# Optimization experiments

Hardware: AMD Instinct MI355X
Metric: run time of the kernel (lower is better)

Reference implementation:

```python
import jax, jax.numpy as jnp
import numpy as np

D = 1024        # d_model
H = 16          # n_heads
DF = 4096       # d_ff
MAXL = 1024     # max_len
MAXSTEPS = 24   # max_steps


def setup_inputs() -> dict:
    key = jax.random.key(0)
    ks = jax.random.split(key, 10)
    B, S = 4, 1024
    s = 0.02
    f32 = jnp.float32
    return {
        "x": jax.random.normal(ks[0], (B, S, D), f32),
        "original_input": jax.random.normal(ks[1], (B, S, D), f32),
        "think_step": 5,
        "step_embed": jax.random.normal(ks[2], (MAXSTEPS, D), f32) * s,
        "Wqkv": jax.random.normal(ks[3], (D, 3 * D), f32) * s,
        "bqkv": jnp.zeros((3 * D,), f32),
        "Wout": jax.random.normal(ks[4], (D, D), f32) * s,
        "bout": jnp.zeros((D,), f32),
        "Wg": jax.random.normal(ks[5], (2 * D, D), f32) * s,
        "bg": jnp.zeros((D,), f32),
        "rel_pos_bias": jax.random.normal(ks[6], (2 * MAXL - 1,), f32) * s,
        "W1": jax.random.normal(ks[7], (D, DF), f32) * s,
        "b1": jnp.zeros((DF,), f32),
        "W2": jax.random.normal(ks[8], (DF, D), f32) * s,
        "b2": jnp.zeros((D,), f32),
        "ln1_g": jnp.ones((D,), f32),
        "ln1_b": jnp.zeros((D,), f32),
        "ln2_g": jnp.ones((D,), f32),
        "ln2_b": jnp.zeros((D,), f32),
    }


def _layer_norm(x, g, b, eps=1e-5):
    m = jnp.mean(x, axis=-1, keepdims=True)
    v = jnp.mean((x - m) ** 2, axis=-1, keepdims=True)
    return (x - m) * jax.lax.rsqrt(v + eps) * g + b


def reference(x, original_input, think_step, step_embed, Wqkv, bqkv, Wout, bout,
              Wg, bg, rel_pos_bias, W1, b1, W2, b2, ln1_g, ln1_b, ln2_g, ln2_b):
    B, S, _ = x.shape
    hd = D // H
    # gated residual input injection
    gate = jax.nn.sigmoid(jnp.concatenate([x, original_input], axis=-1) @ Wg + bg)
    x = x * (1.0 - gate) + original_input * gate
    # think-step embedding (clamped)
    step = min(int(think_step), MAXSTEPS - 1)
    x = x + step_embed[step][None, None, :]
    # qkv projection -> (3, B, H, S, hd)
    qkv = (x @ Wqkv + bqkv).reshape(B, S, 3, H, hd).transpose(2, 0, 3, 1, 4)
    q, k, v = qkv[0], qkv[1], qkv[2]
    scores = jnp.einsum('bhqd,bhkd->bhqk', q, k) * (hd ** -0.5)
    # relative position bias: dist clamped to [0, 2*MAXL-2]
    pos = jnp.arange(S)
    rel = jnp.clip(pos[:, None] - pos[None, :] + (MAXL - 1), 0, 2 * MAXL - 2)
    scores = scores + rel_pos_bias[rel][None, None]  # (B,H,S,S)
    probs = jax.nn.softmax(scores, axis=-1)
    attn = jnp.einsum('bhqk,bhkd->bhqd', probs, v)
    attn = attn.transpose(0, 2, 1, 3).reshape(B, S, D)
    attn = attn @ Wout + bout
    x = _layer_norm(x + attn, ln1_g, ln1_b)
    h = jax.nn.gelu(x @ W1 + b1, approximate=False) @ W2 + b2
    return _layer_norm(x + h, ln2_g, ln2_b)
```

## Files before the change

### kernel.cpp

```cpp
#include <hip/hip_runtime.h>
#include <hip/hip_bf16.h>
#include <math.h>

#define D_MODEL 1024
#define NH      16
#define HD      64
#define DFF     4096
#define SEQ     1024
#define BATCH   4
#define TOK     (BATCH*SEQ)
#define MAXSTEPS 24

typedef __hip_bfloat16 bf16;
typedef __attribute__((ext_vector_type(8))) short short8;
typedef __attribute__((ext_vector_type(4))) float floatx4;

__device__ __forceinline__ float b2f(bf16 v){ return __bfloat162float(v); }
__device__ __forceinline__ bf16  f2b(float v){ return __float2bfloat16(v); }

__device__ __forceinline__ void gload_lds16(const bf16* g, bf16* l){
    __builtin_amdgcn_global_load_lds((const __attribute__((address_space(1))) void*)g,
                                     (__attribute__((address_space(3))) void*)l, 16, 0, 0);
}

template<int TN, int EPI>
__global__ __launch_bounds__(256)
void mfma_gemm(const bf16* __restrict__ A, const bf16* __restrict__ Bt,
               const float* __restrict__ bias, void* __restrict__ outv,
               int M, int N, int K)
{
    constexpr int NT = TN / 32;
    __shared__ bf16 As[128 * 32];
    __shared__ bf16 Bs[TN * 32];
    const int tid  = threadIdx.x;
    const int lane = tid & 63;
    const int w    = tid >> 6;
    const int wm   = w & 1, wn = w >> 1;
    const int fr   = lane & 15;
    const int q    = lane >> 4;
    const int row0 = blockIdx.y * 128, col0 = blockIdx.x * TN;

    floatx4 acc[4][NT] = {};

    for (int k0 = 0; k0 < K; k0 += 32) {
        __syncthreads();
        #pragma unroll
        for (int p = 0; p < 2; ++p) {
            int s  = p * 256 + tid;
            int m  = s >> 2;
            int qg = (s & 3) ^ ((m >> 1) & 3);
            gload_lds16(A + (size_t)(row0 + m) * K + k0 + qg * 8, As + (size_t)s * 8);
        }
        #pragma unroll
        for (int p = 0; p < TN / 64; ++p) {
            int s  = p * 256 + tid;
            int m  = s >> 2;
            int qg = (s & 3) ^ ((m >> 1) & 3);
            gload_lds16(Bt + (size_t)(col0 + m) * K + k0 + qg * 8, Bs + (size_t)s * 8);
        }
        __syncthreads();

        short8 af[4], bfg[NT];
        #pragma unroll
        for (int t = 0; t < 4; ++t) {
            int ml = wm * 64 + t * 16 + fr;
            af[t]  = *(const short8*)(As + (size_t)(ml * 4 + (q ^ ((ml >> 1) & 3))) * 8);
        }
        #pragma unroll
        for (int t = 0; t < NT; ++t) {
            int nl = wn * (TN / 2) + t * 16 + fr;
            bfg[t] = *(const short8*)(Bs + (size_t)(nl * 4 + (q ^ ((nl >> 1) & 3))) * 8);
        }
        #pragma unroll
        for (int i = 0; i < 4; ++i)
            #pragma unroll
            for (int j = 0; j < NT; ++j)
                acc[i][j] = __builtin_amdgcn_mfma_f32_16x16x32_bf16(af[i], bfg[j], acc[i][j], 0, 0, 0);
    }

    float bv[NT];
    #pragma unroll
    for (int nt = 0; nt < NT; ++nt) bv[nt] = bias[col0 + wn * (TN / 2) + nt * 16 + fr];
    #pragma unroll
    for (int mt = 0; mt < 4; ++mt) {
        #pragma unroll
        for (int nt = 0; nt < NT; ++nt) {
            int col = col0 + wn * (TN / 2) + nt * 16 + fr;
            #pragma unroll
            for (int r = 0; r < 4; ++r) {
                int row = row0 + wm * 64 + mt * 16 + q * 4 + r;
                float v = acc[mt][nt][r] + bv[nt];
                if (EPI == 0) {
                    ((float*)outv)[(size_t)row * N + col] = v;
                } else if (EPI == 1) {
                    ((bf16*)outv)[(size_t)row * N + col] = f2b(v);
                } else {
                    float g = 0.5f * v * (1.0f + erff(v * 0.70710678118654752f));
                    ((bf16*)outv)[(size_t)row * N + col] = f2b(g);
                }
            }
        }
    }
}

__global__ __launch_bounds__(256)
void transpose_kernel(const float* __restrict__ W, bf16* __restrict__ WT,
                      int K, int N)
{
    __shared__ float t[32][33];
    const int tx = threadIdx.x & 31, ty = threadIdx.x >> 5;
    const int n0 = blockIdx.x * 32, k0 = blockIdx.y * 32;
    #pragma unroll
    for (int i = 0; i < 4; ++i)
        t[ty + i * 8][tx] = W[(size_t)(k0 + ty + i * 8) * N + n0 + tx];
    __syncthreads();
    #pragma unroll
    for (int i = 0; i < 4; ++i)
        WT[(size_t)(n0 + ty + i * 8) * K + k0 + tx] = f2b(t[tx][ty + i * 8]);
}

__global__ __launch_bounds__(256)
void vtrans_kernel(const bf16* __restrict__ qkv, bf16* __restrict__ Vt)
{
    __shared__ float t[32][33];
    const int blk = blockIdx.x;
    const int dt = blk & 1;
    const int st = (blk >> 1) & 31;
    const int h  = (blk >> 6) & 15;
    const int b  = blk >> 10;
    const int tx = threadIdx.x & 31, ty = threadIdx.x >> 5;
    #pragma unroll
    for (int i = 0; i < 4; ++i)
        t[ty + i * 8][tx] = b2f(qkv[(size_t)(b * SEQ + st * 32 + ty + i * 8) * 3072
                                    + 2048 + h * 64 + dt * 32 + tx]);
    __syncthreads();
    #pragma unroll
    for (int i = 0; i < 4; ++i)
        Vt[(size_t)((b * NH + h) * 64 + dt * 32 + ty + i * 8) * SEQ + st * 32 + tx]
            = f2b(t[tx][ty + i * 8]);
}

__global__ __launch_bounds__(256)
void xcat_kernel(const float* __restrict__ x, const float* __restrict__ orig,
                 bf16* __restrict__ xcat)
{
    int i = blockIdx.x * 256 + threadIdx.x;
    float4 xv = ((const float4*)x)[i];
    float4 ov = ((const float4*)orig)[i];
    int t = i >> 8, c4 = (i & 255) * 4;
    bf16* px = xcat + (size_t)t * 2048 + c4;
    px[0] = f2b(xv.x); px[1] = f2b(xv.y); px[2] = f2b(xv.z); px[3] = f2b(xv.w);
    bf16* po = px + 1024;
    po[0] = f2b(ov.x); po[1] = f2b(ov.y); po[2] = f2b(ov.z); po[3] = f2b(ov.w);
}

__global__ __launch_bounds__(256)
void gatemix_kernel(const float* __restrict__ x, const float* __restrict__ orig,
                    const float* __restrict__ z, const int* __restrict__ step_ptr,
                    const float* __restrict__ se, bf16* __restrict__ xw)
{
    int i = blockIdx.x * 256 + threadIdx.x;
    int st = step_ptr[0];
    st = st < 0 ? 0 : (st > MAXSTEPS - 1 ? MAXSTEPS - 1 : st);
    float g = 1.0f / (1.0f + expf(-z[i]));
    float v = x[i] * (1.0f - g) + orig[i] * g + se[st * D_MODEL + (i & 1023)];
    xw[i] = f2b(v);
}

__global__ __launch_bounds__(256)
void fattn_kernel(const bf16* __restrict__ qkv, const bf16* __restrict__ Vt,
                  const float* __restrict__ relb, bf16* __restrict__ out)
{
    __shared__ bf16 KPs[128 * 64];
    __shared__ bf16 Vs [64 * 128];

    const int tid  = threadIdx.x;
    const int lane = tid & 63;
    const int w    = tid >> 6;
    const int fr   = lane & 15;
    const int quad = lane >> 4;

    const int qt = blockIdx.x & 15;
    const int h  = (blockIdx.x >> 4) & 15;
    const int b  = blockIdx.x >> 8;
    const int bq = b * SEQ;
    const int bh = b * NH + h;

    const int qrow = bq + qt * 64 + w * 16 + fr;
    short8 qf[2];
    {
        const bf16* qp = qkv + (size_t)qrow * 3072 + h * 64 + quad * 8;
        qf[0] = *(const short8*)(qp);
        qf[1] = *(const short8*)(qp + 32);
    }

    float m_run[4], l_run[4];
    floatx4 accO[4];
    #pragma unroll
    for (int r = 0; r < 4; ++r) { m_run[r] = -1e30f; l_run[r] = 0.f; }
    #pragma unroll
    for (int nt = 0; nt < 4; ++nt) accO[nt] = (floatx4){0.f, 0.f, 0.f, 0.f};

    for (int k0 = 0; k0 < SEQ; k0 += 128) {
        __syncthreads();
        #pragma unroll
        for (int it = 0; it < 4; ++it) {
            int s = it * 256 + tid;
            int key = s >> 3, cs = s & 7;
            int c = cs ^ (key & 7);
            const bf16* src = qkv + (size_t)(bq + k0 + key) * 3072 + 1024 + h * 64 + c * 8;
            gload_lds16(src, KPs + (size_t)s * 8);
        }
        #pragma unroll
        for (int it = 0; it < 4; ++it) {
            int s = it * 256 + tid;
            int row = s >> 4, cs = s & 15;
            int c = cs ^ (row & 15);
            const bf16* src = Vt + (size_t)(bh * 64 + row) * SEQ + k0 + c * 8;
            gload_lds16(src, Vs + (size_t)s * 8);
        }
        __syncthreads();

        floatx4 accS[8];
        #pragma unroll
        for (int t = 0; t < 8; ++t) accS[t] = (floatx4){0.f, 0.f, 0.f, 0.f};
        #pragma unroll
        for (int t = 0; t < 8; ++t) {
            int row = t * 16 + fr;
            #pragma unroll
            for (int ks = 0; ks < 2; ++ks) {
                int slot = (ks * 4 + quad) ^ (row & 7);
                short8 kf = *(const short8*)(KPs + (size_t)row * 64 + slot * 8);
                accS[t] = __builtin_amdgcn_mfma_f32_16x16x32_bf16(qf[ks], kf, accS[t], 0, 0, 0);
            }
        }

        float sv[8][4], mloc[4];
        #pragma unroll
        for (int r = 0; r < 4; ++r) mloc[r] = -1e30f;
        #pragma unroll
        for (int t = 0; t < 8; ++t) {
            int kj = k0 + t * 16 + fr;
            #pragma unroll
            for (int r = 0; r < 4; ++r) {
                int qi = qt * 64 + w * 16 + quad * 4 + r;
                float v = accS[t][r] * 0.125f + relb[qi - kj + (SEQ - 1)];
                sv[t][r] = v;
                mloc[r] = fmaxf(mloc[r], v);
            }
        }
        #pragma unroll
        for (int r = 0; r < 4; ++r) {
            float v = mloc[r];
            v = fmaxf(v, __shfl_xor(v, 1));
            v = fmaxf(v, __shfl_xor(v, 2));
            v = fmaxf(v, __shfl_xor(v, 4));
            v = fmaxf(v, __shfl_xor(v, 8));
            mloc[r] = v;
        }
        float alpha[4], lloc[4];
        #pragma unroll
        for (int r = 0; r < 4; ++r) {
            float mn = fmaxf(m_run[r], mloc[r]);
            alpha[r] = expf(m_run[r] - mn);
            m_run[r] = mn;
            lloc[r] = 0.f;
        }

        __syncthreads();

        bf16* Ps = KPs + w * 2048;
        #pragma unroll
        for (int t = 0; t < 8; ++t) {
            int keyl = t * 16 + fr;
            int cbase = keyl >> 3, koff = keyl & 7;
            #pragma unroll
            for (int r = 0; r < 4; ++r) {
                float p = expf(sv[t][r] - m_run[r]);
                lloc[r] += p;
                int row = quad * 4 + r;
                int slot = cbase ^ (row & 15);
                Ps[(size_t)row * 128 + slot * 8 + koff] = f2b(p);
            }
        }
        #pragma unroll
        for (int r = 0; r < 4; ++r) {
            float v = lloc[r];
            v += __shfl_xor(v, 1); v += __shfl_xor(v, 2);
            v += __shfl_xor(v, 4); v += __shfl_xor(v, 8);
            l_run[r] = l_run[r] * alpha[r] + v;
        }
        #pragma unroll
        for (int nt = 0; nt < 4; ++nt)
            #pragma unroll
            for (int r = 0; r < 4; ++r) accO[nt][r] *= alpha[r];

        #pragma unroll
        for (int ks = 0; ks < 4; ++ks) {
            int slotp = (ks * 4 + quad) ^ (fr & 15);
            short8 pf = *(const short8*)(Ps + (size_t)fr * 128 + slotp * 8);
            #pragma unroll
            for (int nt = 0; nt < 4; ++nt) {
                int vrow = nt * 16 + fr;
                int slotv = (ks * 4 + quad) ^ (vrow & 15);
                short8 vf = *(const short8*)(Vs + (size_t)vrow * 128 + slotv * 8);
                accO[nt] = __builtin_amdgcn_mfma_f32_16x16x32_bf16(pf, vf, accO[nt], 0, 0, 0);
            }
        }
    }

    #pragma unroll
    for (int nt = 0; nt < 4; ++nt) {
        int col = h * 64 + nt * 16 + fr;
        #pragma unroll
        for (int r = 0; r < 4; ++r) {
            int t = bq + qt * 64 + w * 16 + quad * 4 + r;
            out[(size_t)t * D_MODEL + col] = f2b(accO[nt][r] / l_run[r]);
        }
    }
}

template<bool OUT_BF16>
__global__ __launch_bounds__(256)
void ln_kernel(const bf16* __restrict__ a, const float* __restrict__ add,
               const float* __restrict__ g, const float* __restrict__ bb,
               void* __restrict__ outv)
{
    __shared__ float red[256];
    __shared__ float red2[256];
    const int row = blockIdx.x;
    const int tid = threadIdx.x;
    float s[4];
    float lsum = 0.f, lsq = 0.f;
    #pragma unroll
    for (int u = 0; u < 4; ++u) {
        int i = tid + 256 * u;
        float v = b2f(a[row * D_MODEL + i]) + add[row * D_MODEL + i];
        s[u] = v; lsum += v; lsq += v * v;
    }
    red[tid] = lsum; red2[tid] = lsq; __syncthreads();
    for (int s2 = 128; s2 > 0; s2 >>= 1) {
        if (tid < s2) { red[tid] += red[tid + s2]; red2[tid] += red2[tid + s2]; }
        __syncthreads();
    }
    float mean = red[0] * (1.0f / D_MODEL);
    float var  = red2[0] * (1.0f / D_MODEL) - mean * mean;
    float rs = rsqrtf(var + 1e-5f);
    #pragma unroll
    for (int u = 0; u < 4; ++u) {
        int i = tid + 256 * u;
        float o = (s[u] - mean) * rs * g[i] + bb[i];
        if (OUT_BF16) ((bf16*)outv)[row * D_MODEL + i] = f2b(o);
        else          ((float*)outv)[row * D_MODEL + i] = o;
    }
}

extern "C" void kernel_launch(void* const* d_in, const int* in_sizes, int n_in,
                              void* d_out, int out_size, void* d_ws, size_t ws_size,
                              hipStream_t stream)
{
    const float* x     = (const float*)d_in[0];
    const float* orig  = (const float*)d_in[1];
    const int*   step  = (const int*)  d_in[2];
    const float* se    = (const float*)d_in[3];
    const float* Wqkv  = (const float*)d_in[4];
    const float* bqkv  = (const float*)d_in[5];
    const float* Wout  = (const float*)d_in[6];
    const float* bout  = (const float*)d_in[7];
    const float* Wg    = (const float*)d_in[8];
    const float* bg    = (const float*)d_in[9];
    const float* relb  = (const float*)d_in[10];
    const float* W1    = (const float*)d_in[11];
    const float* b1    = (const float*)d_in[12];
    const float* W2    = (const float*)d_in[13];
    const float* b2    = (const float*)d_in[14];
    const float* ln1g  = (const float*)d_in[15];
    const float* ln1b  = (const float*)d_in[16];
    const float* ln2g  = (const float*)d_in[17];
    const float* ln2b  = (const float*)d_in[18];

    char* ws = (char*)d_ws;
    bf16* WgT   = (bf16*)(ws);
    bf16* WqkvT = (bf16*)(ws + ( 4u << 20));
    bf16* WoutT = (bf16*)(ws + (10u << 20));
    bf16* W1T   = (bf16*)(ws + (12u << 20));
    bf16* W2T   = (bf16*)(ws + (20u << 20));
    bf16* xcat  = (bf16*)(ws + (28u << 20));
    bf16* xw    = (bf16*)(ws + (28u << 20));
    bf16* attnb = (bf16*)(ws + (36u << 20));
    bf16* qkvb  = (bf16*)(ws + (44u << 20));
    bf16* Vt    = (bf16*)(ws + (68u << 20));
    bf16* h     = (bf16*)(ws + (44u << 20));
    float* tmp  = (float*)d_out;

    dim3 blk(256);

    transpose_kernel<<<dim3(1024/32, 2048/32), blk, 0, stream>>>(Wg,   WgT,   2048, 1024);
    transpose_kernel<<<dim3(3072/32, 1024/32), blk, 0, stream>>>(Wqkv, WqkvT, 1024, 3072);
    transpose_kernel<<<dim3(1024/32, 1024/32), blk, 0, stream>>>(Wout, WoutT, 1024, 1024);
    transpose_kernel<<<dim3(4096/32, 1024/32), blk, 0, stream>>>(W1,   W1T,   1024, 4096);
    transpose_kernel<<<dim3(1024/32, 4096/32), blk, 0, stream>>>(W2,   W2T,   4096, 1024);
    xcat_kernel<<<TOK, blk, 0, stream>>>(x, orig, xcat);

    mfma_gemm<64, 0><<<dim3(D_MODEL/64, TOK/128), blk, 0, stream>>>(
        xcat, WgT, bg, tmp, TOK, D_MODEL, 2*D_MODEL);

    gatemix_kernel<<<TOK*D_MODEL/256, blk, 0, stream>>>(x, orig, tmp, step, se, xw);

    mfma_gemm<128, 1><<<dim3(3*D_MODEL/128, TOK/128), blk, 0, stream>>>(
        xw, WqkvT, bqkv, qkvb, TOK, 3*D_MODEL, D_MODEL);

    vtrans_kernel<<<BATCH*NH*64, blk, 0, stream>>>(qkvb, Vt);

    fattn_kernel<<<BATCH*NH*(SEQ/64), blk, 0, stream>>>(qkvb, Vt, relb, attnb);

    mfma_gemm<64, 0><<<dim3(D_MODEL/64, TOK/128), blk, 0, stream>>>(
        attnb, WoutT, bout, tmp, TOK, D_MODEL, D_MODEL);

    ln_kernel<true><<<TOK, blk, 0, stream>>>(xw, tmp, ln1g, ln1b, xw);

    mfma_gemm<128, 2><<<dim3(DFF/128, TOK/128), blk, 0, stream>>>(
        xw, W1T, b1, h, TOK, DFF, D_MODEL);

    mfma_gemm<64, 0><<<dim3(D_MODEL/64, TOK/128), blk, 0, stream>>>(
        h, W2T, b2, tmp, TOK, D_MODEL, DFF);

    ln_kernel<false><<<TOK, blk, 0, stream>>>(xw, tmp, ln2g, ln2b, d_out);
}
```

Measured before the change: 513.0 us.

## Double-buffer GEMM LDS tiles and swizzle workgroup order for L2 reuse

Turns the MFMA GEMM main loop into a two-stage pipeline: the next K-slice is loaded into a second LDS buffer while the current slice feeds the MFMAs, so each iteration needs one barrier instead of two. Workgroup IDs are remapped into bands of 8 row-tiles, grouped by bid&7, to improve L2 reuse of A and B tiles. Global and LDS address offsets are now computed once before the loop. The cost is double the shared memory, which may lower occupancy, and the remap assumes the tile count divides by 8.

```diff
diff --git a/kernel.cpp b/kernel.cpp
--- a/kernel.cpp
+++ b/kernel.cpp
@@ -29,53 +29,86 @@
                const float* __restrict__ bias, void* __restrict__ outv,
                int M, int N, int K)
 {
-    constexpr int NT = TN / 32;
-    __shared__ bf16 As[128 * 32];
-    __shared__ bf16 Bs[TN * 32];
+    constexpr int NT  = TN / 32;
+    constexpr int NBP = TN / 64;
+    __shared__ bf16 As[2][128 * 32];
+    __shared__ bf16 Bs[2][TN * 32];
     const int tid  = threadIdx.x;
     const int lane = tid & 63;
     const int w    = tid >> 6;
     const int wm   = w & 1, wn = w >> 1;
     const int fr   = lane & 15;
     const int q    = lane >> 4;
-    const int row0 = blockIdx.y * 128, col0 = blockIdx.x * TN;
+
+    const int tn_g = gridDim.x;
+    const int nwg  = tn_g * gridDim.y;
+    const int bid  = blockIdx.y * tn_g + blockIdx.x;
+    const int o    = (bid & 7) * (nwg >> 3) + (bid >> 3);
+    const int bandw = 8 * tn_g;
+    const int band  = o / bandw;
+    const int rr    = o - band * bandw;
+    const int row0 = (band * 8 + (rr & 7)) * 128;
+    const int col0 = (rr >> 3) * TN;
+
+    const bf16* gA[2]; int sA_[2];
+    #pragma unroll
+    for (int p = 0; p < 2; ++p) {
+        int s  = p * 256 + tid;
+        int m  = s >> 2;
+        int qg = (s & 3) ^ ((m >> 1) & 3);
+        gA[p]  = A + (size_t)(row0 + m) * K + qg * 8;
+        sA_[p] = s * 8;
+    }
+    const bf16* gB[NBP]; int sB_[NBP];
+    #pragma unroll
+    for (int p = 0; p < NBP; ++p) {
+        int s  = p * 256 + tid;
+        int m  = s >> 2;
+        int qg = (s & 3) ^ ((m >> 1) & 3);
+        gB[p]  = Bt + (size_t)(col0 + m) * K + qg * 8;
+        sB_[p] = s * 8;
+    }
+
+    int aoff[4], boff[NT];
+    #pragma unroll
+    for (int t = 0; t < 4; ++t) {
+        int ml  = wm * 64 + t * 16 + fr;
+        aoff[t] = (ml * 4 + (q ^ ((ml >> 1) & 3))) * 8;
+    }
+    #pragma unroll
+    for (int t = 0; t < NT; ++t) {
+        int nl  = wn * (TN / 2) + t * 16 + fr;
+        boff[t] = (nl * 4 + (q ^ ((nl >> 1) & 3))) * 8;
+    }
+
+    #pragma unroll
+    for (int p = 0; p < 2; ++p)   gload_lds16(gA[p], &As[0][sA_[p]]);
+    #pragma unroll
+    for (int p = 0; p < NBP; ++p) gload_lds16(gB[p], &Bs[0][sB_[p]]);
 
     floatx4 acc[4][NT] = {};
-
-    for (int k0 = 0; k0 < K; k0 += 32) {
-        __syncthreads();
-        #pragma unroll
-        for (int p = 0; p < 2; ++p) {
-            int s  = p * 256 + tid;
-            int m  = s >> 2;
-            int qg = (s & 3) ^ ((m >> 1) & 3);
-            gload_lds16(A + (size_t)(row0 + m) * K + k0 + qg * 8, As + (size_t)s * 8);
-        }
-        #pragma unroll
-        for (int p = 0; p < TN / 64; ++p) {
-            int s  = p * 256 + tid;
-            int m  = s >> 2;
-            int qg = (s & 3) ^ ((m >> 1) & 3);
-            gload_lds16(Bt + (size_t)(col0 + m) * K + k0 + qg * 8, Bs + (size_t)s * 8);
-        }
-        __syncthreads();
-
+    __syncthreads();
+
+    int cur = 0;
+    for (int k0 = 32; k0 <= K; k0 += 32) {
+        if (k0 < K) {
+            #pragma unroll
+            for (int p = 0; p < 2; ++p)   gload_lds16(gA[p] + k0, &As[cur ^ 1][sA_[p]]);
+            #pragma unroll
+            for (int p = 0; p < NBP; ++p) gload_lds16(gB[p] + k0, &Bs[cur ^ 1][sB_[p]]);
+        }
         short8 af[4], bfg[NT];
         #pragma unroll
-        for (int t = 0; t < 4; ++t) {
-            int ml = wm * 64 + t * 16 + fr;
-            af[t]  = *(const short8*)(As + (size_t)(ml * 4 + (q ^ ((ml >> 1) & 3))) * 8);
-        }
-        #pragma unroll
-        for (int t = 0; t < NT; ++t) {
-            int nl = wn * (TN / 2) + t * 16 + fr;
-            bfg[t] = *(const short8*)(Bs + (size_t)(nl * 4 + (q ^ ((nl >> 1) & 3))) * 8);
-        }
+        for (int t = 0; t < 4; ++t)  af[t]  = *(const short8*)(&As[cur][aoff[t]]);
+        #pragma unroll
+        for (int t = 0; t < NT; ++t) bfg[t] = *(const short8*)(&Bs[cur][boff[t]]);
         #pragma unroll
         for (int i = 0; i < 4; ++i)
             #pragma unroll
             for (int j = 0; j < NT; ++j)
                 acc[i][j] = __builtin_amdgcn_mfma_f32_16x16x32_bf16(af[i], bfg[j], acc[i][j], 0, 0, 0);
+        __syncthreads();
+        cur ^= 1;
     }
 
     float bv[NT];
```

After: 475.6 us. -7.3%, faster.
